# Kernel tuning notes

Measured on AMD Instinct MI355X. Metric: run time of the kernel, lower is better.

The kernel has to match this reference:

```python
import jax, jax.numpy as jnp
import numpy as np

B, S, D = 4, 4096, 2048
DQ = D // 4          # router hidden
DF = 4 * D           # layer_fn FFN hidden
CAPACITY = 0.125


def setup_inputs() -> dict:
    key = jax.random.key(0)
    ks = jax.random.split(key, 5)
    sc = 0.02
    return {
        "x":   jax.random.normal(ks[0], (B, S, D), jnp.float32),
        "Wr1": jax.random.normal(ks[1], (D, DQ), jnp.float32) * sc,
        "br1": jnp.zeros((DQ,), jnp.float32),
        "Wr2": jax.random.normal(ks[2], (DQ, 1), jnp.float32) * sc,
        "br2": jnp.zeros((1,), jnp.float32),
        "Wf1": jax.random.normal(ks[3], (D, DF), jnp.float32) * sc,
        "bf1": jnp.zeros((DF,), jnp.float32),
        "Wf2": jax.random.normal(ks[4], (DF, D), jnp.float32) * sc,
        "bf2": jnp.zeros((D,), jnp.float32),
    }


def reference(x, Wr1, br1, Wr2, br2, Wf1, bf1, Wf2, bf2):
    b, s, d = x.shape
    k = max(1, int(CAPACITY * s))

    # router: Linear -> ReLU -> Linear -> squeeze(-1)
    h = jax.nn.relu(jnp.einsum("bsd,dq->bsq", x, Wr1) + br1)
    scores = (jnp.einsum("bsq,qo->bso", h, Wr2) + br2)[..., 0]   # [B, S]

    # top-k token selection per batch row
    topk_scores, topk_idx = jax.lax.top_k(scores, k)             # [B, k]

    # gather selected tokens
    sel = jnp.take_along_axis(x, topk_idx[..., None], axis=1)    # [B, k, D]

    # layer_fn: standard FFN (D -> 4D -> D) on selected tokens only
    proc = jnp.einsum("bkf,fd->bkd",
                      jax.nn.relu(jnp.einsum("bkd,df->bkf", sel, Wf1) + bf1),
                      Wf2) + bf2                                 # [B, k, D]

    # scatter processed tokens back into a copy of x
    batch_idx = jnp.arange(b)[:, None]                           # [B, 1]
    output = x.at[batch_idx, topk_idx].set(proc)                 # [B, S, D]

    mask = jnp.zeros((b, s), dtype=bool).at[batch_idx, topk_idx].set(True)
    return output, mask
```

## Files before the change

kernel.cpp:

```cpp
#include <hip/hip_runtime.h>

#define B_    4
#define S_    4096
#define D_    2048
#define DQ_   512
#define DF_   8192
#define KSEL_ 512
#define M_    (B_ * S_)
#define MS_   (B_ * KSEL_)

typedef __attribute__((ext_vector_type(8))) short bf16x8;
typedef __attribute__((ext_vector_type(4))) float f32x4;
typedef __attribute__((address_space(3))) void as3_void;
typedef const __attribute__((address_space(1))) void as1_cvoid;

__device__ __forceinline__ unsigned short f2bf(float f) {
    unsigned u = __float_as_uint(f);
    u += 0x7FFFu + ((u >> 16) & 1u);
    return (unsigned short)(u >> 16);
}
__device__ __forceinline__ float bf2f(unsigned short h) {
    return __uint_as_float(((unsigned)h) << 16);
}

__device__ __forceinline__ void gload16(const void* g, void* l) {
    __builtin_amdgcn_global_load_lds((as1_cvoid*)g, (as3_void*)l, 16, 0, 0);
}

__global__ void split_copy_kernel(const float* __restrict__ x,
                                  unsigned short* __restrict__ xh,
                                  unsigned short* __restrict__ xl,
                                  float* __restrict__ out, int n8) {
    int i = blockIdx.x * blockDim.x + threadIdx.x;
    int stride = gridDim.x * blockDim.x;
    for (; i < n8; i += stride) {
        float4 a = ((const float4*)x)[2 * i];
        float4 b = ((const float4*)x)[2 * i + 1];
        ((float4*)out)[2 * i]     = a;
        ((float4*)out)[2 * i + 1] = b;
        float v[8] = {a.x, a.y, a.z, a.w, b.x, b.y, b.z, b.w};
        unsigned short hi[8], lo[8];
#pragma unroll
        for (int j = 0; j < 8; j++) {
            hi[j] = f2bf(v[j]);
            lo[j] = f2bf(v[j] - bf2f(hi[j]));
        }
        *(uint4*)(xh + (size_t)i * 8) = *(const uint4*)hi;
        *(uint4*)(xl + (size_t)i * 8) = *(const uint4*)lo;
    }
}

__global__ void wsplit_kernel(const float* __restrict__ W,
                              unsigned short* __restrict__ whiT,
                              unsigned short* __restrict__ wloT) {
    __shared__ float tile[32][33];
    int tx = threadIdx.x, ty = threadIdx.y;
    int n0 = blockIdx.x * 32, k0 = blockIdx.y * 32;
#pragma unroll
    for (int j = 0; j < 4; j++)
        tile[ty + j * 8][tx] = W[(size_t)(k0 + ty + j * 8) * DQ_ + n0 + tx];
    __syncthreads();
#pragma unroll
    for (int j = 0; j < 4; j++) {
        float v = tile[tx][ty + j * 8];
        unsigned short hi = f2bf(v);
        unsigned short lo = f2bf(v - bf2f(hi));
        size_t row = (size_t)(n0 + ty + j * 8) * D_;
        whiT[row + k0 + tx] = hi;
        wloT[row + k0 + tx] = lo;
    }
}

__global__ void transpose_bf16_kernel(const float* __restrict__ in,
                                      unsigned short* __restrict__ out,
                                      int R, int C) {
    __shared__ float tile[32][33];
    int tx = threadIdx.x, ty = threadIdx.y;
    int c0 = blockIdx.x * 32, r0 = blockIdx.y * 32;
#pragma unroll
    for (int j = 0; j < 4; j++)
        tile[ty + j * 8][tx] = in[(size_t)(r0 + ty + j * 8) * C + c0 + tx];
    __syncthreads();
#pragma unroll
    for (int j = 0; j < 4; j++)
        out[(size_t)(c0 + ty + j * 8) * R + r0 + tx] = f2bf(tile[tx][ty + j * 8]);
}

#define RSTAGE(bufp, ktX) do {                                              \
    const size_t ko_ = (size_t)(ktX) * 32;                                  \
    char* laH_ = (char*)(&sA[bufp][0][0]) + w * 1024;                       \
    char* laL_ = (char*)(&sA[bufp][1][0]) + w * 1024;                       \
    char* lbH_ = (char*)(&sB[bufp][0][0]) + w * 1024;                       \
    char* lbL_ = (char*)(&sB[bufp][1][0]) + w * 1024;                       \
    gload16(gAh + ko_,            laH_);                                    \
    gload16(gAh + 64 * D_ + ko_,  laH_ + 4096);                             \
    gload16(gAl + ko_,            laL_);                                    \
    gload16(gAl + 64 * D_ + ko_,  laL_ + 4096);                             \
    gload16(gBh + ko_,            lbH_);                                    \
    gload16(gBh + 64 * D_ + ko_,  lbH_ + 4096);                             \
    gload16(gBl + ko_,            lbL_);                                    \
    gload16(gBl + 64 * D_ + ko_,  lbL_ + 4096);                             \
  } while (0)

__global__ __launch_bounds__(256) void router_mfma(const unsigned short* __restrict__ xh,
                                                   const unsigned short* __restrict__ xl,
                                                   const unsigned short* __restrict__ whiT,
                                                   const unsigned short* __restrict__ wloT,
                                                   const float* __restrict__ br1,
                                                   const float* __restrict__ Wr2,
                                                   float* __restrict__ pscore) {
    __shared__ unsigned short sA[2][2][128 * 32];
    __shared__ unsigned short sB[2][2][128 * 32];
    const int t = threadIdx.x;
    const int w = t >> 6, l = t & 63;
    const int m0 = blockIdx.x * 128, n0 = blockIdx.y * 128;
    const int wr = w >> 1, wc = w & 1;

    f32x4 acc[4][4];
    const f32x4 zz = {0.f, 0.f, 0.f, 0.f};
#pragma unroll
    for (int m = 0; m < 4; m++)
#pragma unroll
        for (int n = 0; n < 4; n++) acc[m][n] = zz;

    const int srow = t >> 2;
    const int sch8 = (((t & 3) ^ ((t >> 3) & 3)) * 8);
    const unsigned short* gAh = xh + (size_t)(m0 + srow) * D_ + sch8;
    const unsigned short* gAl = xl + (size_t)(m0 + srow) * D_ + sch8;
    const unsigned short* gBh = whiT + (size_t)(n0 + srow) * D_ + sch8;
    const unsigned short* gBl = wloT + (size_t)(n0 + srow) * D_ + sch8;

    RSTAGE(0, 0);
    RSTAGE(1, 1);

    const int fro = ((l >> 4) ^ ((l >> 1) & 3)) * 8;
    const int arB = (wr * 64 + (l & 15)) * 32 + fro;
    const int brB = (wc * 64 + (l & 15)) * 32 + fro;

    for (int kt = 0; kt < 64; ++kt) {
        if (kt + 1 < 64) { asm volatile("s_waitcnt vmcnt(8)" ::: "memory"); }
        else             { asm volatile("s_waitcnt vmcnt(0)" ::: "memory"); }
        __builtin_amdgcn_s_barrier();
        __builtin_amdgcn_sched_barrier(0);
        const int cur = kt & 1;
        const unsigned short* LAh = &sA[cur][0][0];
        const unsigned short* LAl = &sA[cur][1][0];
        const unsigned short* LBh = &sB[cur][0][0];
        const unsigned short* LBl = &sB[cur][1][0];
        bf16x8 ah[4], al[4], bh[4], bl[4];
#pragma unroll
        for (int f = 0; f < 4; f++) {
            ah[f] = *(const bf16x8*)(LAh + arB + f * 512);
            bh[f] = *(const bf16x8*)(LBh + brB + f * 512);
            bl[f] = *(const bf16x8*)(LBl + brB + f * 512);
            al[f] = *(const bf16x8*)(LAl + arB + f * 512);
        }
        __builtin_amdgcn_s_setprio(1);
#pragma unroll
        for (int m = 0; m < 4; m++)
#pragma unroll
            for (int n = 0; n < 4; n++)
                acc[m][n] = __builtin_amdgcn_mfma_f32_16x16x32_bf16(ah[m], bh[n], acc[m][n], 0, 0, 0);
#pragma unroll
        for (int m = 0; m < 4; m++)
#pragma unroll
            for (int n = 0; n < 4; n++)
                acc[m][n] = __builtin_amdgcn_mfma_f32_16x16x32_bf16(ah[m], bl[n], acc[m][n], 0, 0, 0);
#pragma unroll
        for (int m = 0; m < 4; m++)
#pragma unroll
            for (int n = 0; n < 4; n++)
                acc[m][n] = __builtin_amdgcn_mfma_f32_16x16x32_bf16(al[m], bh[n], acc[m][n], 0, 0, 0);
        __builtin_amdgcn_s_setprio(0);
        __builtin_amdgcn_sched_barrier(0);
        __builtin_amdgcn_s_barrier();
        if (kt + 2 < 64) RSTAGE(cur, kt + 2);
    }

    float br1v[4], wr2v[4];
#pragma unroll
    for (int nf = 0; nf < 4; nf++) {
        int col = n0 + wc * 64 + nf * 16 + (l & 15);
        br1v[nf] = br1[col];
        wr2v[nf] = Wr2[col];
    }
#pragma unroll
    for (int mf = 0; mf < 4; mf++)
#pragma unroll
        for (int q = 0; q < 4; q++) {
            float s = 0.f;
#pragma unroll
            for (int nf = 0; nf < 4; nf++)
                s += fmaxf(acc[mf][nf][q] + br1v[nf], 0.f) * wr2v[nf];
#pragma unroll
            for (int off = 8; off >= 1; off >>= 1)
                s += __shfl_xor(s, off);
            if ((l & 15) == 0) {
                int row = m0 + wr * 64 + mf * 16 + (l >> 4) * 4 + q;
                pscore[(size_t)(blockIdx.y * 2 + wc) * M_ + row] = s;
            }
        }
}

__global__ __launch_bounds__(1024) void topk_kernel(const float* __restrict__ pscore,
                                                    const float* __restrict__ br2,
                                                    int* __restrict__ sel_idx,
                                                    float* __restrict__ maskF) {
    __shared__ unsigned long long keys[S_];
    __shared__ unsigned char flags[S_];
    int b = blockIdx.x, t = threadIdx.x;
    float bb = br2[0];
    for (int i = t; i < S_; i += 1024) {
        int m = b * S_ + i;
        float f = bb;
#pragma unroll
        for (int s8 = 0; s8 < 8; s8++) f += pscore[(size_t)s8 * M_ + m];
        unsigned u = __float_as_uint(f);
        u = (u & 0x80000000u) ? ~u : (u | 0x80000000u);
        keys[i] = ((unsigned long long)u << 32) | (unsigned)(S_ - 1 - i);
        flags[i] = 0;
    }
    __syncthreads();
    for (int k = 2; k <= S_; k <<= 1)
        for (int j = k >> 1; j > 0; j >>= 1) {
            for (int i = t; i < S_; i += 1024) {
                int l = i ^ j;
                if (l > i) {
                    unsigned long long a = keys[i], c = keys[l];
                    bool up = ((i & k) == 0);
                    if (up ? (a > c) : (a < c)) { keys[i] = c; keys[l] = a; }
                }
            }
            __syncthreads();
        }
    for (int i = t; i < KSEL_; i += 1024) {
        unsigned long long kk = keys[S_ - KSEL_ + i];
        int s = (S_ - 1) - (int)(kk & 0xFFFFFFFFu);
        sel_idx[b * KSEL_ + i] = s;
        flags[s] = 1;
    }
    __syncthreads();
    for (int i = t; i < S_; i += 1024)
        maskF[b * S_ + i] = flags[i] ? 1.0f : 0.0f;
}

__global__ void gather_kernel(const float* __restrict__ x, const int* __restrict__ sel_idx,
                              unsigned short* __restrict__ sel) {
    int jrow = blockIdx.x;
    int b = jrow >> 9;
    int tok = sel_idx[jrow];
    const float* src = x + ((size_t)(b * S_ + tok)) * D_;
    int t = threadIdx.x;
    float4 v0 = ((const float4*)src)[2 * t];
    float4 v1 = ((const float4*)src)[2 * t + 1];
    unsigned p0 = (unsigned)f2bf(v0.x) | ((unsigned)f2bf(v0.y) << 16);
    unsigned p1 = (unsigned)f2bf(v0.z) | ((unsigned)f2bf(v0.w) << 16);
    unsigned p2 = (unsigned)f2bf(v1.x) | ((unsigned)f2bf(v1.y) << 16);
    unsigned p3 = (unsigned)f2bf(v1.z) | ((unsigned)f2bf(v1.w) << 16);
    *(uint4*)(sel + (size_t)jrow * D_ + t * 8) = make_uint4(p0, p1, p2, p3);
}

#define STAGEAB(bufp, ktX) do {                                                   \
    const unsigned short* a_ = gA + (size_t)(ktX) * 64;                           \
    const unsigned short* b_ = gB + (size_t)(ktX) * 64;                           \
    char* la_ = (char*)(&lds[bufp][0][0]) + w * 1024;                             \
    char* lb_ = (char*)(&lds[bufp][1][0]) + w * 1024;                             \
    gload16(a_,                      la_);                                        \
    gload16(a_ +  64 * (size_t)K,    la_ + 8192);                                 \
    gload16(a_ + 128 * (size_t)K,    la_ + 16384);                                \
    gload16(a_ + 192 * (size_t)K,    la_ + 24576);                                \
    gload16(b_,                      lb_);                                        \
    gload16(b_ +  64 * (size_t)K,    lb_ + 8192);                                 \
    gload16(b_ + 128 * (size_t)K,    lb_ + 16384);                                \
    gload16(b_ + 192 * (size_t)K,    lb_ + 24576);                                \
  } while (0)

__global__ __launch_bounds__(512) void mfma_gemm256(const unsigned short* __restrict__ A,
                                                    const unsigned short* __restrict__ Bt,
                                                    int M, int N, int K, int kspan,
                                                    const float* __restrict__ bias,
                                                    unsigned short* __restrict__ Cbf,
                                                    float* __restrict__ partial,
                                                    int epi) {
    __shared__ unsigned short lds[2][2][256 * 64];
    const int t = threadIdx.x;
    const int w = t >> 6, l = t & 63;
    const int m0 = blockIdx.y * 256, n0 = blockIdx.x * 256;
    const int wr = w >> 2, wc = w & 3;
    const int kbeg = blockIdx.z * kspan;
    const int NT = kspan / 64;

    f32x4 acc[8][4];
    const f32x4 zz = {0.f, 0.f, 0.f, 0.f};
#pragma unroll
    for (int m = 0; m < 8; m++)
#pragma unroll
        for (int n = 0; n < 4; n++) acc[m][n] = zz;

    const int srow = t >> 3;
    const int sch8 = (((t & 7) ^ ((t >> 3) & 7)) * 8);
    const unsigned short* gA = A + (size_t)(m0 + srow) * K + kbeg + sch8;
    const unsigned short* gB = Bt + (size_t)(n0 + srow) * K + kbeg + sch8;

    STAGEAB(0, 0);
    STAGEAB(1, 1);

    for (int kt = 0; kt < NT; ++kt) {
        if (kt + 1 < NT) { asm volatile("s_waitcnt vmcnt(8)" ::: "memory"); }
        else             { asm volatile("s_waitcnt vmcnt(0)" ::: "memory"); }
        __builtin_amdgcn_s_barrier();
        __builtin_amdgcn_sched_barrier(0);
        const int cur = kt & 1;
        const unsigned short* LA = &lds[cur][0][0];
        const unsigned short* LB = &lds[cur][1][0];
#pragma unroll
        for (int kk = 0; kk < 2; kk++) {
            const int sw_ = ((kk * 4 + (l >> 4)) ^ (l & 7)) * 8;
            bf16x8 bfr[4], af0[4], af1[4];
#pragma unroll
            for (int n = 0; n < 4; n++)
                bfr[n] = *(const bf16x8*)(LB + (wc * 64 + n * 16 + (l & 15)) * 64 + sw_);
#pragma unroll
            for (int m = 0; m < 4; m++) {
                af0[m] = *(const bf16x8*)(LA + (wr * 128 + m * 16 + (l & 15)) * 64 + sw_);
                af1[m] = *(const bf16x8*)(LA + (wr * 128 + 64 + m * 16 + (l & 15)) * 64 + sw_);
            }
            __builtin_amdgcn_s_setprio(1);
#pragma unroll
            for (int m = 0; m < 4; m++)
#pragma unroll
                for (int n = 0; n < 4; n++)
                    acc[m][n] = __builtin_amdgcn_mfma_f32_16x16x32_bf16(af0[m], bfr[n], acc[m][n], 0, 0, 0);
#pragma unroll
            for (int m = 0; m < 4; m++)
#pragma unroll
                for (int n = 0; n < 4; n++)
                    acc[4 + m][n] = __builtin_amdgcn_mfma_f32_16x16x32_bf16(af1[m], bfr[n], acc[4 + m][n], 0, 0, 0);
            __builtin_amdgcn_s_setprio(0);
        }
        __builtin_amdgcn_sched_barrier(0);
        __builtin_amdgcn_s_barrier();
        if (kt + 2 < NT) STAGEAB(cur, kt + 2);
    }

    if (epi == 0) {
#pragma unroll
        for (int m = 0; m < 8; m++) {
            int rowb = m0 + wr * 128 + m * 16 + (l >> 4) * 4;
#pragma unroll
            for (int n = 0; n < 4; n++) {
                int col = n0 + wc * 64 + n * 16 + (l & 15);
                float bv = bias[col];
#pragma unroll
                for (int q = 0; q < 4; q++) {
                    float v = fmaxf(acc[m][n][q] + bv, 0.f);
                    Cbf[(size_t)(rowb + q) * N + col] = f2bf(v);
                }
            }
        }
    } else {
        float* pseg = partial + (size_t)blockIdx.z * M * N;
#pragma unroll
        for (int m = 0; m < 8; m++) {
            int rowb = m0 + wr * 128 + m * 16 + (l >> 4) * 4;
#pragma unroll
            for (int n = 0; n < 4; n++) {
                int col = n0 + wc * 64 + n * 16 + (l & 15);
#pragma unroll
                for (int q = 0; q < 4; q++)
                    pseg[(size_t)(rowb + q) * N + col] = acc[m][n][q];
            }
        }
    }
}

__global__ void reduce_scatter_kernel(const float* __restrict__ partial,
                                      const float* __restrict__ bias,
                                      const int* __restrict__ sel_idx,
                                      float* __restrict__ out) {
    int m = blockIdx.x;
    int t = threadIdx.x;
    int brow = m >> 9;
    int tok = sel_idx[m];
    float* orow = out + ((size_t)(brow * S_ + tok)) * D_;
    const float* p0 = partial + (size_t)m * D_;
    const size_t seg = (size_t)MS_ * D_;
#pragma unroll
    for (int r = 0; r < 2; r++) {
        int c = (t + r * 256) * 4;
        float4 v0 = *(const float4*)(p0 + c);
        float4 v1 = *(const float4*)(p0 + seg + c);
        float4 v2 = *(const float4*)(p0 + 2 * seg + c);
        float4 v3 = *(const float4*)(p0 + 3 * seg + c);
        float4 bv = *(const float4*)(bias + c);
        float4 o;
        o.x = v0.x + v1.x + v2.x + v3.x + bv.x;
        o.y = v0.y + v1.y + v2.y + v3.y + bv.y;
        o.z = v0.z + v1.z + v2.z + v3.z + bv.z;
        o.w = v0.w + v1.w + v2.w + v3.w + bv.w;
        *(float4*)(orow + c) = o;
    }
}

extern "C" void kernel_launch(void* const* d_in, const int* in_sizes, int n_in,
                              void* d_out, int out_size, void* d_ws, size_t ws_size,
                              hipStream_t stream) {
    const float* x   = (const float*)d_in[0];
    const float* Wr1 = (const float*)d_in[1];
    const float* br1 = (const float*)d_in[2];
    const float* Wr2 = (const float*)d_in[3];
    const float* br2 = (const float*)d_in[4];
    const float* Wf1 = (const float*)d_in[5];
    const float* bf1 = (const float*)d_in[6];
    const float* Wf2 = (const float*)d_in[7];
    const float* bf2 = (const float*)d_in[8];
    float* out = (float*)d_out;
    char* ws = (char*)d_ws;

    unsigned short* xh   = (unsigned short*)(ws);
    unsigned short* xl   = (unsigned short*)(ws + (64u << 20));
    unsigned short* whiT = (unsigned short*)(ws + (160u << 20));
    unsigned short* wloT = (unsigned short*)(ws + (162u << 20));
    float* pscore        = (float*)(ws + (168u << 20));
    int* sel_idx         = (int*)(ws + (169u << 20));
    float* partial       = (float*)(ws);
    unsigned short* w1t  = (unsigned short*)(ws + (64u << 20));
    unsigned short* w2t  = (unsigned short*)(ws + (96u << 20));
    unsigned short* h1   = (unsigned short*)(ws + (128u << 20));
    unsigned short* sel  = (unsigned short*)(ws + (160u << 20));
    float* maskF         = out + (size_t)B_ * S_ * D_;

    (void)in_sizes; (void)n_in; (void)out_size; (void)ws_size;

    split_copy_kernel<<<2048, 256, 0, stream>>>(x, xh, xl, out, (M_ * D_) / 8);
    wsplit_kernel<<<dim3(DQ_ / 32, D_ / 32), dim3(32, 8), 0, stream>>>(Wr1, whiT, wloT);
    router_mfma<<<dim3(M_ / 128, DQ_ / 128), 256, 0, stream>>>(
        xh, xl, whiT, wloT, br1, Wr2, pscore);
    topk_kernel<<<B_, 1024, 0, stream>>>(pscore, br2, sel_idx, maskF);
    gather_kernel<<<MS_, 256, 0, stream>>>(x, sel_idx, sel);
    transpose_bf16_kernel<<<dim3(DF_ / 32, D_ / 32), dim3(32, 8), 0, stream>>>(Wf1, w1t, D_, DF_);
    transpose_bf16_kernel<<<dim3(D_ / 32, DF_ / 32), dim3(32, 8), 0, stream>>>(Wf2, w2t, DF_, D_);
    mfma_gemm256<<<dim3(DF_ / 256, MS_ / 256, 1), 512, 0, stream>>>(
        sel, w1t, MS_, DF_, D_, D_, bf1, h1, nullptr, 0);
    mfma_gemm256<<<dim3(D_ / 256, MS_ / 256, 4), 512, 0, stream>>>(
        h1, w2t, MS_, D_, DF_, DF_ / 4, nullptr, nullptr, partial, 1);
    reduce_scatter_kernel<<<MS_, 256, 0, stream>>>(partial, bf2, sel_idx, out);
}
```

Before: 441.2 us.

## Shrink router GEMM M-tile to 64 and drop LDS double buffering

The router GEMM tile is halved in M (128 to 64 rows per block), which doubles the grid and halves the accumulators per wave. The double-buffered async LDS pipeline with manual vmcnt waits is replaced by a single buffer that loads and then syncs each k-step. The aim is more blocks and occupancy across CUs, at the cost of losing load/compute overlap, adding two barriers per iteration, and lowering B-tile reuse.

```diff
diff --git a/kernel.cpp b/kernel.cpp
--- a/kernel.cpp
+++ b/kernel.cpp
@@ -86,20 +86,14 @@
         out[(size_t)(c0 + ty + j * 8) * R + r0 + tx] = f2bf(tile[tx][ty + j * 8]);
 }
 
-#define RSTAGE(bufp, ktX) do {                                              \
+#define RSTAGE(ktX) do {                                                    \
     const size_t ko_ = (size_t)(ktX) * 32;                                  \
-    char* laH_ = (char*)(&sA[bufp][0][0]) + w * 1024;                       \
-    char* laL_ = (char*)(&sA[bufp][1][0]) + w * 1024;                       \
-    char* lbH_ = (char*)(&sB[bufp][0][0]) + w * 1024;                       \
-    char* lbL_ = (char*)(&sB[bufp][1][0]) + w * 1024;                       \
-    gload16(gAh + ko_,            laH_);                                    \
-    gload16(gAh + 64 * D_ + ko_,  laH_ + 4096);                             \
-    gload16(gAl + ko_,            laL_);                                    \
-    gload16(gAl + 64 * D_ + ko_,  laL_ + 4096);                             \
-    gload16(gBh + ko_,            lbH_);                                    \
-    gload16(gBh + 64 * D_ + ko_,  lbH_ + 4096);                             \
-    gload16(gBl + ko_,            lbL_);                                    \
-    gload16(gBl + 64 * D_ + ko_,  lbL_ + 4096);                             \
+    gload16(gAh + ko_,            (char*)sAh + w * 1024);                   \
+    gload16(gAl + ko_,            (char*)sAl + w * 1024);                   \
+    gload16(gBh + ko_,            (char*)sBh + w * 1024);                   \
+    gload16(gBh + 64 * D_ + ko_,  (char*)sBh + 4096 + w * 1024);            \
+    gload16(gBl + ko_,            (char*)sBl + w * 1024);                   \
+    gload16(gBl + 64 * D_ + ko_,  (char*)sBl + 4096 + w * 1024);            \
   } while (0)
 
 __global__ __launch_bounds__(256) void router_mfma(const unsigned short* __restrict__ xh,
@@ -109,17 +103,19 @@
                                                    const float* __restrict__ br1,
                                                    const float* __restrict__ Wr2,
                                                    float* __restrict__ pscore) {
-    __shared__ unsigned short sA[2][2][128 * 32];
-    __shared__ unsigned short sB[2][2][128 * 32];
+    __shared__ unsigned short sAh[64 * 32];
+    __shared__ unsigned short sAl[64 * 32];
+    __shared__ unsigned short sBh[128 * 32];
+    __shared__ unsigned short sBl[128 * 32];
     const int t = threadIdx.x;
     const int w = t >> 6, l = t & 63;
-    const int m0 = blockIdx.x * 128, n0 = blockIdx.y * 128;
+    const int m0 = blockIdx.x * 64, n0 = blockIdx.y * 128;
     const int wr = w >> 1, wc = w & 1;
 
-    f32x4 acc[4][4];
+    f32x4 acc[2][4];
     const f32x4 zz = {0.f, 0.f, 0.f, 0.f};
 #pragma unroll
-    for (int m = 0; m < 4; m++)
+    for (int m = 0; m < 2; m++)
 #pragma unroll
         for (int n = 0; n < 4; n++) acc[m][n] = zz;
 
@@ -130,51 +126,42 @@
     const unsigned short* gBh = whiT + (size_t)(n0 + srow) * D_ + sch8;
     const unsigned short* gBl = wloT + (size_t)(n0 + srow) * D_ + sch8;
 
-    RSTAGE(0, 0);
-    RSTAGE(1, 1);
-
     const int fro = ((l >> 4) ^ ((l >> 1) & 3)) * 8;
-    const int arB = (wr * 64 + (l & 15)) * 32 + fro;
+    const int arB = (wr * 32 + (l & 15)) * 32 + fro;
     const int brB = (wc * 64 + (l & 15)) * 32 + fro;
 
     for (int kt = 0; kt < 64; ++kt) {
-        if (kt + 1 < 64) { asm volatile("s_waitcnt vmcnt(8)" ::: "memory"); }
-        else             { asm volatile("s_waitcnt vmcnt(0)" ::: "memory"); }
-        __builtin_amdgcn_s_barrier();
-        __builtin_amdgcn_sched_barrier(0);
-        const int cur = kt & 1;
-        const unsigned short* LAh = &sA[cur][0][0];
-        const unsigned short* LAl = &sA[cur][1][0];
-        const unsigned short* LBh = &sB[cur][0][0];
-        const unsigned short* LBl = &sB[cur][1][0];
-        bf16x8 ah[4], al[4], bh[4], bl[4];
+        RSTAGE(kt);
+        __syncthreads();
+        bf16x8 ah[2], al[2], bh[4], bl[4];
+#pragma unroll
+        for (int f = 0; f < 2; f++) {
+            ah[f] = *(const bf16x8*)(sAh + arB + f * 512);
+            al[f] = *(const bf16x8*)(sAl + arB + f * 512);
+        }
 #pragma unroll
         for (int f = 0; f < 4; f++) {
-            ah[f] = *(const bf16x8*)(LAh + arB + f * 512);
-            bh[f] = *(const bf16x8*)(LBh + brB + f * 512);
-            bl[f] = *(const bf16x8*)(LBl + brB + f * 512);
-            al[f] = *(const bf16x8*)(LAl + arB + f * 512);
+            bh[f] = *(const bf16x8*)(sBh + brB + f * 512);
+            bl[f] = *(const bf16x8*)(sBl + brB + f * 512);
         }
         __builtin_amdgcn_s_setprio(1);
 #pragma unroll
-        for (int m = 0; m < 4; m++)
+        for (int m = 0; m < 2; m++)
 #pragma unroll
             for (int n = 0; n < 4; n++)
                 acc[m][n] = __builtin_amdgcn_mfma_f32_16x16x32_bf16(ah[m], bh[n], acc[m][n], 0, 0, 0);
 #pragma unroll
-        for (int m = 0; m < 4; m++)
+        for (int m = 0; m < 2; m++)
 #pragma unroll
             for (int n = 0; n < 4; n++)
                 acc[m][n] = __builtin_amdgcn_mfma_f32_16x16x32_bf16(ah[m], bl[n], acc[m][n], 0, 0, 0);
 #pragma unroll
-        for (int m = 0; m < 4; m++)
+        for (int m = 0; m < 2; m++)
 #pragma unroll
             for (int n = 0; n < 4; n++)
                 acc[m][n] = __builtin_amdgcn_mfma_f32_16x16x32_bf16(al[m], bh[n], acc[m][n], 0, 0, 0);
         __builtin_amdgcn_s_setprio(0);
-        __builtin_amdgcn_sched_barrier(0);
-        __builtin_amdgcn_s_barrier();
-        if (kt + 2 < 64) RSTAGE(cur, kt + 2);
+        __syncthreads();
     }
 
     float br1v[4], wr2v[4];
@@ -185,7 +172,7 @@
         wr2v[nf] = Wr2[col];
     }
 #pragma unroll
-    for (int mf = 0; mf < 4; mf++)
+    for (int mf = 0; mf < 2; mf++)
 #pragma unroll
         for (int q = 0; q < 4; q++) {
             float s = 0.f;
@@ -196,7 +183,7 @@
             for (int off = 8; off >= 1; off >>= 1)
                 s += __shfl_xor(s, off);
             if ((l & 15) == 0) {
-                int row = m0 + wr * 64 + mf * 16 + (l >> 4) * 4 + q;
+                int row = m0 + wr * 32 + mf * 16 + (l >> 4) * 4 + q;
                 pscore[(size_t)(blockIdx.y * 2 + wc) * M_ + row] = s;
             }
         }
@@ -434,7 +421,7 @@
 
     split_copy_kernel<<<2048, 256, 0, stream>>>(x, xh, xl, out, (M_ * D_) / 8);
     wsplit_kernel<<<dim3(DQ_ / 32, D_ / 32), dim3(32, 8), 0, stream>>>(Wr1, whiT, wloT);
-    router_mfma<<<dim3(M_ / 128, DQ_ / 128), 256, 0, stream>>>(
+    router_mfma<<<dim3(M_ / 64, DQ_ / 128), 256, 0, stream>>>(
         xh, xl, whiT, wloT, br1, Wr2, pscore);
     topk_kernel<<<B_, 1024, 0, stream>>>(pscore, br2, sel_idx, maskF);
     gather_kernel<<<MS_, 256, 0, stream>>>(x, sel_idx, sel);
```

New measurement: 493.6 us. +11.9%, slower.
